# Kernel tuning notes

Measured on AMD Instinct MI355X. Metric: run time of the kernel, lower is better.

## Reference

```python
import jax, jax.numpy as jnp
from jax import lax
import numpy as np

T = 8  # num_temp_tokens (init kwarg, closed over as a static constant)


def setup_inputs() -> dict:
    key = jax.random.key(0)
    k1, k2, k3, k4, k5 = jax.random.split(key, 5)
    B, N, C = 16, 197, 768
    bt = B * T
    x = jax.random.normal(k1, (bt, N, C), dtype=jnp.float32)
    # routing conv1d: C -> 3C, kernel 3 (original inits to zero; small random for testing)
    a_weight = jax.random.normal(k2, (3 * C, C, 3), dtype=jnp.float32) * 0.02
    a_bias = jax.random.normal(k3, (3 * C,), dtype=jnp.float32) * 0.02
    # main linear weight (out_channels=3C, in_channels=C) and bias
    weight = jax.random.normal(k4, (3 * C, C), dtype=jnp.float32) * 0.02
    bias = jax.random.normal(k5, (3 * C,), dtype=jnp.float32) * 0.02
    return {"x": x, "a_weight": a_weight, "a_bias": a_bias, "weight": weight, "bias": bias}


def reference(x, a_weight, a_bias, weight, bias):
    bt, n, c = x.shape
    b = bt // T
    xr = x.reshape(b, T, n, c)                      # (b, t, n, c)
    # routing: conv1d over T on the CLS token, then +1
    cls = jnp.transpose(xr[:, :, 0, :], (0, 2, 1))  # (b, c, t)
    r = lax.conv_general_dilated(
        cls, a_weight, window_strides=(1,), padding=[(1, 1)],
        dimension_numbers=("NCH", "OIH", "NCH"),
    ) + a_bias[None, :, None] + 1.0                 # (b, 3c, t)
    s = jnp.transpose(r, (0, 2, 1)).reshape(b, T, 3, c)   # per-(b,t) q/k/v c_in scales
    Wr = weight.reshape(3, c, c)                    # (3, c_out, c_in)
    br = bias.reshape(3, c)
    # scale input channels per (b, t, group), then batched GEMM
    xs = xr[:, :, None, :, :] * s[:, :, :, None, :]       # (b, t, 3, n, c)
    out = jnp.einsum("goi,btgni->btgon", Wr, xs)          # (b, t, 3, c_out, n)
    out = out + (br[None, None] * s)[..., None]           # bias also modulated by scales
    return out.reshape(bt, 3 * c, n)                # (b*t, 3c, n) == torch output layout
```

## Files before the change

### kernel.cpp

```cpp
#include <hip/hip_runtime.h>

#define NTOK 197
#define C 768
#define C3 2304
#define BM 128
#define BK 32
#define PK 40
#define NT 13

typedef __attribute__((ext_vector_type(4))) float f32x4;
typedef __attribute__((ext_vector_type(8))) short bf16x8;

__device__ __forceinline__ ushort f2bf(float f){
  uint u = __float_as_uint(f);
  u += 0x7fffu + ((u >> 16) & 1u);
  return (ushort)(u >> 16);
}
__device__ __forceinline__ uint pack2(float a, float b){
  return (uint)f2bf(a) | ((uint)f2bf(b) << 16);
}
__device__ __forceinline__ float bfu2f(uint u){ return __uint_as_float(u << 16); }

__global__ __launch_bounds__(256)
void conv_scales(const float* __restrict__ x, const float* __restrict__ aw,
                 const float* __restrict__ ab, float* __restrict__ s_ws)
{
  __shared__ __align__(16) float cls[10][C];
  __shared__ float partial[64][4][8];
  const int oc  = blockIdx.x;
  const int b   = blockIdx.y;
  const int tid = threadIdx.x;

  for (int task = tid; task < 1920; task += 256){
    int row = task / 192, c4 = task % 192;
    float4 v = {0.f,0.f,0.f,0.f};
    if (row >= 1 && row <= 8)
      v = *reinterpret_cast<const float4*>(x + (size_t)(b*8 + row - 1)*NTOK*C + c4*4);
    *reinterpret_cast<float4*>(&cls[row][c4*4]) = v;
  }
  __syncthreads();

  const int ol = tid >> 2, part = tid & 3;
  const int o_full = oc*64 + ol;
  float acc[8];
  #pragma unroll
  for (int t=0;t<8;t++) acc[t]=0.f;
  const float* awrow = aw + (size_t)o_full*2304;

  for (int i = part*192; i < part*192 + 192; i += 4){
    const float* ap = awrow + i*3;
    float4 a0 = *reinterpret_cast<const float4*>(ap);
    float4 a1 = *reinterpret_cast<const float4*>(ap+4);
    float4 a2 = *reinterpret_cast<const float4*>(ap+8);
    float awf[12] = {a0.x,a0.y,a0.z,a0.w, a1.x,a1.y,a1.z,a1.w, a2.x,a2.y,a2.z,a2.w};
    float4 cv[10];
    #pragma unroll
    for (int t=0;t<10;t++) cv[t] = *reinterpret_cast<const float4*>(&cls[t][i]);
    #pragma unroll
    for (int e=0;e<4;e++){
      float w0 = awf[e*3+0], w1 = awf[e*3+1], w2 = awf[e*3+2];
      #pragma unroll
      for (int t=0;t<8;t++){
        const float* c0 = reinterpret_cast<const float*>(&cv[t]);
        const float* c1 = reinterpret_cast<const float*>(&cv[t+1]);
        const float* c2 = reinterpret_cast<const float*>(&cv[t+2]);
        acc[t] += w0*c0[e] + w1*c1[e] + w2*c2[e];
      }
    }
  }
  #pragma unroll
  for (int t=0;t<8;t++) partial[ol][part][t] = acc[t];
  __syncthreads();

  for (int idx = tid; idx < 512; idx += 256){
    int o_l = idx >> 3, t = idx & 7;
    float v = partial[o_l][0][t] + partial[o_l][1][t]
            + partial[o_l][2][t] + partial[o_l][3][t]
            + ab[oc*64 + o_l] + 1.0f;
    s_ws[(size_t)(b*8 + t)*C3 + oc*64 + o_l] = v;
  }
}

__global__ void cvt_bf16(const float* __restrict__ in, ushort* __restrict__ outp, int n4)
{
  int stride = gridDim.x * blockDim.x;
  for (int i = blockIdx.x*blockDim.x + threadIdx.x; i < n4; i += stride){
    float4 v = reinterpret_cast<const float4*>(in)[i];
    ushort4 o;
    o.x = f2bf(v.x); o.y = f2bf(v.y); o.z = f2bf(v.z); o.w = f2bf(v.w);
    reinterpret_cast<ushort4*>(outp)[i] = o;
  }
}

template<bool XBF>
__global__ __launch_bounds__(512)
void gemm_kernel(const float* __restrict__ x, const ushort* __restrict__ xbf,
                 const ushort* __restrict__ wbf, const float* __restrict__ s_ws,
                 const float* __restrict__ bias, float* __restrict__ out)
{
  __shared__ __align__(16) ushort A_lds[BM*PK];
  __shared__ __align__(16) ushort B_lds[208*PK];
  const int ot  = blockIdx.x;
  const int g   = blockIdx.y;
  const int bt  = blockIdx.z;
  const int tid = threadIdx.x;
  const int w = tid >> 6, lane = tid & 63;
  const int l15 = lane & 15, lq = lane >> 4;

  const float*  srow  = s_ws + (size_t)bt*C3 + (size_t)g*C;
  const ushort* wrow  = wbf + ((size_t)g*C + (size_t)ot*BM)*C;
  const float*  xrow  = x   + (size_t)bt*NTOK*C;
  const ushort* xbrow = xbf + (size_t)bt*NTOK*C;

  f32x4 acc[NT];
  #pragma unroll
  for (int j=0;j<NT;j++) acc[j] = (f32x4){0.f,0.f,0.f,0.f};

  const int ar = tid >> 2, ac = tid & 3;

  for (int k0 = 0; k0 < C; k0 += BK){
    {
      uint4 wv = *reinterpret_cast<const uint4*>(wrow + (size_t)ar*C + k0 + ac*8);
      const float* sv = srow + k0 + ac*8;
      float4 s0 = *reinterpret_cast<const float4*>(sv);
      float4 s1 = *reinterpret_cast<const float4*>(sv+4);
      uint4 av;
      av.x = pack2(bfu2f(wv.x & 0xffffu)*s0.x, bfu2f(wv.x >> 16)*s0.y);
      av.y = pack2(bfu2f(wv.y & 0xffffu)*s0.z, bfu2f(wv.y >> 16)*s0.w);
      av.z = pack2(bfu2f(wv.z & 0xffffu)*s1.x, bfu2f(wv.z >> 16)*s1.y);
      av.w = pack2(bfu2f(wv.w & 0xffffu)*s1.z, bfu2f(wv.w >> 16)*s1.w);
      *reinterpret_cast<uint4*>(&A_lds[ar*PK + ac*8]) = av;
    }
    #pragma unroll
    for (int it = 0; it < 2; ++it){
      int task = tid + it*512;
      if (task < 832){
        int r = task >> 2, cc = task & 3;
        uint4 bv = {0u,0u,0u,0u};
        if (r < NTOK){
          if (XBF){
            bv = *reinterpret_cast<const uint4*>(xbrow + (size_t)r*C + k0 + cc*8);
          } else {
            const float* p = xrow + (size_t)r*C + k0 + cc*8;
            float4 lo = *reinterpret_cast<const float4*>(p);
            float4 hi = *reinterpret_cast<const float4*>(p+4);
            bv.x = pack2(lo.x, lo.y); bv.y = pack2(lo.z, lo.w);
            bv.z = pack2(hi.x, hi.y); bv.w = pack2(hi.z, hi.w);
          }
        }
        *reinterpret_cast<uint4*>(&B_lds[r*PK + cc*8]) = bv;
      }
    }
    __syncthreads();

    bf16x8 a = *reinterpret_cast<const bf16x8*>(&A_lds[(w*16 + l15)*PK + lq*8]);
    #pragma unroll
    for (int j=0;j<NT;j++){
      bf16x8 b = *reinterpret_cast<const bf16x8*>(&B_lds[(j*16 + l15)*PK + lq*8]);
      acc[j] = __builtin_amdgcn_mfma_f32_16x16x32_bf16(a, b, acc[j], 0, 0, 0);
    }
    __syncthreads();
  }

  const int obase = ot*BM + w*16 + lq*4;
  float bs[4];
  #pragma unroll
  for (int r=0;r<4;r++)
    bs[r] = bias[g*C + obase + r] * srow[obase + r];
  #pragma unroll
  for (int j=0;j<NT;j++){
    int n = j*16 + l15;
    if (n < NTOK){
      #pragma unroll
      for (int r=0;r<4;r++)
        out[((size_t)bt*C3 + g*C + obase + r)*NTOK + n] = acc[j][r] + bs[r];
    }
  }
}

extern "C" void kernel_launch(void* const* d_in, const int* in_sizes, int n_in,
                              void* d_out, int out_size, void* d_ws, size_t ws_size,
                              hipStream_t stream)
{
  const float* x        = (const float*)d_in[0];
  const float* a_weight = (const float*)d_in[1];
  const float* a_bias   = (const float*)d_in[2];
  const float* weight   = (const float*)d_in[3];
  const float* bias     = (const float*)d_in[4];
  float* out = (float*)d_out;

  char* ws = (char*)d_ws;
  float*  s_ws = (float*)ws;
  ushort* wbf  = (ushort*)(ws + 1179648);
  ushort* xbf  = (ushort*)(ws + 4718592);
  const bool use_xbf = ws_size >= (size_t)43450368;

  conv_scales<<<dim3(36,16), 256, 0, stream>>>(x, a_weight, a_bias, s_ws);
  cvt_bf16<<<dim3(1728), 256, 0, stream>>>(weight, wbf, 442368);
  if (use_xbf){
    cvt_bf16<<<dim3(4096), 256, 0, stream>>>(x, xbf, 4841472);
    gemm_kernel<true><<<dim3(6,3,128), 512, 0, stream>>>(x, xbf, wbf, s_ws, bias, out);
  } else {
    gemm_kernel<false><<<dim3(6,3,128), 512, 0, stream>>>(x, xbf, wbf, s_ws, bias, out);
  }
}
```

Before: 563.3 us.

## Pre-scale X into bf16 planes and run one large shared-weight GEMM

Adds a scale_x pass that multiplies x by the per-(bt,group) routing scales and writes three padded bf16 planes. A new 128x128-tile MFMA GEMM then treats all bt×token columns as one large N dimension, so a single bf16 weight copy is reused across the batch instead of being rescaled per bt. The GEMM fills LDS with direct global-to-LDS loads. The routing conv also switches to bf16-converted weights staged in LDS. The cost is a large workspace requirement and an extra write and read of the scaled activation planes. Converting the conv weights to bf16 also slightly reduces the precision of the scales.

```diff
diff --git a/kernel.cpp b/kernel.cpp
--- a/kernel.cpp
+++ b/kernel.cpp
@@ -7,9 +7,13 @@
 #define BK 32
 #define PK 40
 #define NT 13
+#define CPAD 772
+#define AWP 200
+#define XS_PLANE 20447232
 
 typedef __attribute__((ext_vector_type(4))) float f32x4;
 typedef __attribute__((ext_vector_type(8))) short bf16x8;
+typedef unsigned int u32;
 
 __device__ __forceinline__ ushort f2bf(float f){
   uint u = __float_as_uint(f);
@@ -21,15 +25,30 @@
 }
 __device__ __forceinline__ float bfu2f(uint u){ return __uint_as_float(u << 16); }
 
+__device__ __forceinline__ void glds16(ushort* lds, const ushort* gsrc){
+  __builtin_amdgcn_global_load_lds((const __attribute__((address_space(1))) u32*)gsrc,
+                                   (__attribute__((address_space(3))) u32*)lds, 16, 0, 0);
+}
+
+__global__ void cvt_bf16(const float* __restrict__ in, ushort* __restrict__ outp, int n4)
+{
+  int stride = gridDim.x * blockDim.x;
+  for (int i = blockIdx.x*blockDim.x + threadIdx.x; i < n4; i += stride){
+    float4 v = reinterpret_cast<const float4*>(in)[i];
+    ushort4 o;
+    o.x = f2bf(v.x); o.y = f2bf(v.y); o.z = f2bf(v.z); o.w = f2bf(v.w);
+    reinterpret_cast<ushort4*>(outp)[i] = o;
+  }
+}
+
 __global__ __launch_bounds__(256)
-void conv_scales(const float* __restrict__ x, const float* __restrict__ aw,
-                 const float* __restrict__ ab, float* __restrict__ s_ws)
-{
-  __shared__ __align__(16) float cls[10][C];
-  __shared__ float partial[64][4][8];
-  const int oc  = blockIdx.x;
-  const int b   = blockIdx.y;
-  const int tid = threadIdx.x;
+void conv_scales2(const float* __restrict__ x, const ushort* __restrict__ awbf,
+                  const float* __restrict__ ab, float* __restrict__ s_ws)
+{
+  __shared__ __align__(16) float  cls[10][CPAD];
+  __shared__ __align__(16) ushort awt[64*AWP];
+  __shared__ float partial[64][4][9];
+  const int oc = blockIdx.x, b = blockIdx.y, tid = threadIdx.x;
 
   for (int task = tid; task < 1920; task += 256){
     int row = task / 192, c4 = task % 192;
@@ -38,6 +57,186 @@
       v = *reinterpret_cast<const float4*>(x + (size_t)(b*8 + row - 1)*NTOK*C + c4*4);
     *reinterpret_cast<float4*>(&cls[row][c4*4]) = v;
   }
+
+  const int o_l = tid >> 2, part = tid & 3;
+  float acc[8];
+  #pragma unroll
+  for (int t=0;t<8;t++) acc[t]=0.f;
+
+  for (int it = 0; it < 12; ++it){
+    const int i0 = it*64;
+    #pragma unroll
+    for (int j = 0; j < 6; ++j){
+      int task = tid + j*256;
+      int r = task / 24, c8 = task % 24;
+      uint4 v = *reinterpret_cast<const uint4*>(awbf + (size_t)(oc*64 + r)*C3 + i0*3 + c8*8);
+      *reinterpret_cast<uint4*>(&awt[r*AWP + c8*8]) = v;
+    }
+    __syncthreads();
+
+    #pragma unroll
+    for (int qq = 0; qq < 4; ++qq){
+      const int i_loc = part*16 + qq*4;
+      const int ib = i0 + i_loc;
+      float4 cv[10];
+      #pragma unroll
+      for (int t=0;t<10;t++) cv[t] = *reinterpret_cast<const float4*>(&cls[t][ib]);
+      float wv[4][3];
+      #pragma unroll
+      for (int e=0;e<4;e++){
+        #pragma unroll
+        for (int dk=0;dk<3;dk++)
+          wv[e][dk] = bfu2f((uint)awt[o_l*AWP + (i_loc+e)*3 + dk]);
+      }
+      #pragma unroll
+      for (int e=0;e<4;e++){
+        #pragma unroll
+        for (int dk=0;dk<3;dk++){
+          const float wf = wv[e][dk];
+          #pragma unroll
+          for (int t=0;t<8;t++){
+            const float* cp = reinterpret_cast<const float*>(&cv[t+dk]);
+            acc[t] += wf * cp[e];
+          }
+        }
+      }
+    }
+    __syncthreads();
+  }
+
+  #pragma unroll
+  for (int t=0;t<8;t++) partial[o_l][part][t] = acc[t];
+  __syncthreads();
+
+  for (int idx = tid; idx < 512; idx += 256){
+    int o = idx >> 3, t = idx & 7;
+    float v = partial[o][0][t] + partial[o][1][t]
+            + partial[o][2][t] + partial[o][3][t]
+            + ab[oc*64 + o] + 1.0f;
+    s_ws[(size_t)(b*8 + t)*C3 + oc*64 + o] = v;
+  }
+}
+
+__global__ __launch_bounds__(256)
+void scale_x(const float* __restrict__ x, const float* __restrict__ s_ws,
+             ushort* __restrict__ Xs)
+{
+  const int NCH = 128*208*96;
+  int stride = gridDim.x * blockDim.x;
+  for (int idx = blockIdx.x*blockDim.x + threadIdx.x; idx < NCH; idx += stride){
+    int kc = idx % 96;
+    int n  = (idx / 96) % 208;
+    int bt = idx / (96*208);
+    uint4 og[3];
+    #pragma unroll
+    for (int g=0; g<3; g++) og[g] = (uint4){0u,0u,0u,0u};
+    if (n < NTOK){
+      const float* xp = x + ((size_t)bt*NTOK + n)*C + kc*8;
+      float4 xa = *reinterpret_cast<const float4*>(xp);
+      float4 xb = *reinterpret_cast<const float4*>(xp+4);
+      #pragma unroll
+      for (int g=0; g<3; g++){
+        const float* sp = s_ws + (size_t)bt*C3 + g*C + kc*8;
+        float4 sa = *reinterpret_cast<const float4*>(sp);
+        float4 sb = *reinterpret_cast<const float4*>(sp+4);
+        og[g].x = pack2(xa.x*sa.x, xa.y*sa.y);
+        og[g].y = pack2(xa.z*sa.z, xa.w*sa.w);
+        og[g].z = pack2(xb.x*sb.x, xb.y*sb.y);
+        og[g].w = pack2(xb.z*sb.z, xb.w*sb.w);
+      }
+    }
+    size_t base = ((size_t)bt*208 + n)*C + kc*8;
+    #pragma unroll
+    for (int g=0; g<3; g++)
+      *reinterpret_cast<uint4*>(Xs + (size_t)g*XS_PLANE + base) = og[g];
+  }
+}
+
+__global__ __launch_bounds__(256)
+void gemm2(const ushort* __restrict__ wbf, const ushort* __restrict__ Xs,
+           const float* __restrict__ s_ws, const float* __restrict__ bias,
+           float* __restrict__ out)
+{
+  __shared__ __align__(16) ushort A_lds[128*32];
+  __shared__ __align__(16) ushort B_lds[128*32];
+  const int tn = blockIdx.x;
+  const int tm = blockIdx.y;
+  const int g  = blockIdx.z;
+  const int tid = threadIdx.x, w = tid >> 6, lane = tid & 63;
+  const int l15 = lane & 15, lq = lane >> 4;
+  const int wm = w >> 1, wn = w & 1;
+
+  const ushort* Ap = wbf + (size_t)g*C*C + (size_t)(tm*128)*C;
+  const ushort* Bp = Xs  + (size_t)g*XS_PLANE + (size_t)(tn*128)*C;
+
+  const int srow0 = w*32 + (lane >> 2);
+  const int scol  = (lane & 3)*8;
+
+  f32x4 acc[4][4];
+  #pragma unroll
+  for (int i=0;i<4;i++)
+    #pragma unroll
+    for (int j=0;j<4;j++) acc[i][j] = (f32x4){0.f,0.f,0.f,0.f};
+
+  for (int k0 = 0; k0 < C; k0 += BK){
+    glds16(&A_lds[w*1024      ], Ap + (size_t)(srow0     )*C + k0 + scol);
+    glds16(&A_lds[w*1024 + 512], Ap + (size_t)(srow0 + 16)*C + k0 + scol);
+    glds16(&B_lds[w*1024      ], Bp + (size_t)(srow0     )*C + k0 + scol);
+    glds16(&B_lds[w*1024 + 512], Bp + (size_t)(srow0 + 16)*C + k0 + scol);
+    __syncthreads();
+
+    bf16x8 a[4], b[4];
+    #pragma unroll
+    for (int mf=0; mf<4; mf++)
+      a[mf] = *reinterpret_cast<const bf16x8*>(&A_lds[(wm*64 + mf*16 + l15)*BK + lq*8]);
+    #pragma unroll
+    for (int nf=0; nf<4; nf++)
+      b[nf] = *reinterpret_cast<const bf16x8*>(&B_lds[(wn*64 + nf*16 + l15)*BK + lq*8]);
+    #pragma unroll
+    for (int mf=0; mf<4; mf++)
+      #pragma unroll
+      for (int nf=0; nf<4; nf++)
+        acc[mf][nf] = __builtin_amdgcn_mfma_f32_16x16x32_bf16(a[mf], b[nf], acc[mf][nf], 0, 0, 0);
+    __syncthreads();
+  }
+
+  #pragma unroll
+  for (int nf=0; nf<4; nf++){
+    int col = tn*128 + wn*64 + nf*16 + l15;
+    unsigned bt = (unsigned)col / 208u;
+    unsigned n  = (unsigned)col - bt*208u;
+    if (n < NTOK){
+      #pragma unroll
+      for (int mf=0; mf<4; mf++){
+        int o = tm*128 + wm*64 + mf*16 + lq*4;
+        #pragma unroll
+        for (int r=0; r<4; r++){
+          int oo = o + r;
+          float bs = bias[g*C + oo] * s_ws[(size_t)bt*C3 + g*C + oo];
+          out[((size_t)bt*C3 + g*C + oo)*NTOK + n] = acc[mf][nf][r] + bs;
+        }
+      }
+    }
+  }
+}
+
+__global__ __launch_bounds__(256)
+void conv_scales(const float* __restrict__ x, const float* __restrict__ aw,
+                 const float* __restrict__ ab, float* __restrict__ s_ws)
+{
+  __shared__ __align__(16) float cls[10][C];
+  __shared__ float partial[64][4][8];
+  const int oc  = blockIdx.x;
+  const int b   = blockIdx.y;
+  const int tid = threadIdx.x;
+
+  for (int task = tid; task < 1920; task += 256){
+    int row = task / 192, c4 = task % 192;
+    float4 v = {0.f,0.f,0.f,0.f};
+    if (row >= 1 && row <= 8)
+      v = *reinterpret_cast<const float4*>(x + (size_t)(b*8 + row - 1)*NTOK*C + c4*4);
+    *reinterpret_cast<float4*>(&cls[row][c4*4]) = v;
+  }
   __syncthreads();
 
   const int ol = tid >> 2, part = tid & 3;
@@ -45,7 +244,7 @@
   float acc[8];
   #pragma unroll
   for (int t=0;t<8;t++) acc[t]=0.f;
-  const float* awrow = aw + (size_t)o_full*2304;
+  const float* awrow = aw + (size_t)o_full*C3;
 
   for (int i = part*192; i < part*192 + 192; i += 4){
     const float* ap = awrow + i*3;
@@ -81,22 +280,10 @@
   }
 }
 
-__global__ void cvt_bf16(const float* __restrict__ in, ushort* __restrict__ outp, int n4)
-{
-  int stride = gridDim.x * blockDim.x;
-  for (int i = blockIdx.x*blockDim.x + threadIdx.x; i < n4; i += stride){
-    float4 v = reinterpret_cast<const float4*>(in)[i];
-    ushort4 o;
-    o.x = f2bf(v.x); o.y = f2bf(v.y); o.z = f2bf(v.z); o.w = f2bf(v.w);
-    reinterpret_cast<ushort4*>(outp)[i] = o;
-  }
-}
-
-template<bool XBF>
 __global__ __launch_bounds__(512)
-void gemm_kernel(const float* __restrict__ x, const ushort* __restrict__ xbf,
-                 const ushort* __restrict__ wbf, const float* __restrict__ s_ws,
-                 const float* __restrict__ bias, float* __restrict__ out)
+void gemm_fallback(const float* __restrict__ x, const ushort* __restrict__ wbf,
+                   const float* __restrict__ s_ws, const float* __restrict__ bias,
+                   float* __restrict__ out)
 {
   __shared__ __align__(16) ushort A_lds[BM*PK];
   __shared__ __align__(16) ushort B_lds[208*PK];
@@ -110,7 +297,6 @@
   const float*  srow  = s_ws + (size_t)bt*C3 + (size_t)g*C;
   const ushort* wrow  = wbf + ((size_t)g*C + (size_t)ot*BM)*C;
   const float*  xrow  = x   + (size_t)bt*NTOK*C;
-  const ushort* xbrow = xbf + (size_t)bt*NTOK*C;
 
   f32x4 acc[NT];
   #pragma unroll
@@ -138,15 +324,11 @@
         int r = task >> 2, cc = task & 3;
         uint4 bv = {0u,0u,0u,0u};
         if (r < NTOK){
-          if (XBF){
-            bv = *reinterpret_cast<const uint4*>(xbrow + (size_t)r*C + k0 + cc*8);
-          } else {
-            const float* p = xrow + (size_t)r*C + k0 + cc*8;
-            float4 lo = *reinterpret_cast<const float4*>(p);
-            float4 hi = *reinterpret_cast<const float4*>(p+4);
-            bv.x = pack2(lo.x, lo.y); bv.y = pack2(lo.z, lo.w);
-            bv.z = pack2(hi.x, hi.y); bv.w = pack2(hi.z, hi.w);
-          }
+          const float* p = xrow + (size_t)r*C + k0 + cc*8;
+          float4 lo = *reinterpret_cast<const float4*>(p);
+          float4 hi = *reinterpret_cast<const float4*>(p+4);
+          bv.x = pack2(lo.x, lo.y); bv.y = pack2(lo.z, lo.w);
+          bv.z = pack2(hi.x, hi.y); bv.w = pack2(hi.z, hi.w);
         }
         *reinterpret_cast<uint4*>(&B_lds[r*PK + cc*8]) = bv;
       }
@@ -192,15 +374,24 @@
   char* ws = (char*)d_ws;
   float*  s_ws = (float*)ws;
   ushort* wbf  = (ushort*)(ws + 1179648);
-  ushort* xbf  = (ushort*)(ws + 4718592);
-  const bool use_xbf = ws_size >= (size_t)43450368;
-
-  conv_scales<<<dim3(36,16), 256, 0, stream>>>(x, a_weight, a_bias, s_ws);
+  ushort* awbf = (ushort*)(ws + 4718592);
+  ushort* Xs   = (ushort*)(ws + 15335424);
+  const size_t NEED_FULL = 138018816;
+  const size_t NEED_MID  = 15335424;
+
   cvt_bf16<<<dim3(1728), 256, 0, stream>>>(weight, wbf, 442368);
-  if (use_xbf){
-    cvt_bf16<<<dim3(4096), 256, 0, stream>>>(x, xbf, 4841472);
-    gemm_kernel<true><<<dim3(6,3,128), 512, 0, stream>>>(x, xbf, wbf, s_ws, bias, out);
+
+  if (ws_size >= NEED_FULL){
+    cvt_bf16<<<dim3(4096), 256, 0, stream>>>(a_weight, awbf, 1327104);
+    conv_scales2<<<dim3(36,16), 256, 0, stream>>>(x, awbf, a_bias, s_ws);
+    scale_x<<<dim3(2048), 256, 0, stream>>>(x, s_ws, Xs);
+    gemm2<<<dim3(208,6,3), 256, 0, stream>>>(wbf, Xs, s_ws, bias, out);
+  } else if (ws_size >= NEED_MID){
+    cvt_bf16<<<dim3(4096), 256, 0, stream>>>(a_weight, awbf, 1327104);
+    conv_scales2<<<dim3(36,16), 256, 0, stream>>>(x, awbf, a_bias, s_ws);
+    gemm_fallback<<<dim3(6,3,128), 512, 0, stream>>>(x, wbf, s_ws, bias, out);
   } else {
-    gemm_kernel<false><<<dim3(6,3,128), 512, 0, stream>>>(x, xbf, wbf, s_ws, bias, out);
-  }
-}
+    conv_scales<<<dim3(36,16), 256, 0, stream>>>(x, a_weight, a_bias, s_ws);
+    gemm_fallback<<<dim3(6,3,128), 512, 0, stream>>>(x, wbf, s_ws, bias, out);
+  }
+}
```

After: 626.9 us. 11.3% more time.
